# Performance work log

Hardware: AMD Instinct MI355X
Metric: run time of the kernel (lower is better)

The kernel has to match this reference:

```python
import jax, jax.numpy as jnp
import numpy as np

EMBED_DIM = 1024
N_HEADS = 16
HEAD_DIM = EMBED_DIM // N_HEADS


def setup_inputs() -> dict:
    key = jax.random.key(0)
    k_x, k_qw, k_qb, k_ow, k_ob = jax.random.split(key, 5)
    s = 1.0 / np.sqrt(EMBED_DIM)
    return {
        "x": jax.random.normal(k_x, (2, 2048, EMBED_DIM), dtype=jnp.float32),
        "qkv_w": jax.random.uniform(k_qw, (3 * EMBED_DIM, EMBED_DIM), jnp.float32, -s, s),
        "qkv_b": jax.random.uniform(k_qb, (3 * EMBED_DIM,), jnp.float32, -s, s),
        "out_w": jax.random.uniform(k_ow, (EMBED_DIM, EMBED_DIM), jnp.float32, -s, s),
        "out_b": jax.random.uniform(k_ob, (EMBED_DIM,), jnp.float32, -s, s),
    }


def reference(x, qkv_w, qkv_b, out_w, out_b):
    B, S, E = x.shape
    # fused QKV projection (torch Linear: x @ W^T + b)
    qkv = x @ qkv_w.T + qkv_b                      # [B,S,3E]
    qkv = qkv.reshape(B, S, N_HEADS, 3 * HEAD_DIM).transpose(0, 2, 1, 3)  # [B,H,S,3d]
    q, k, v = jnp.split(qkv, 3, axis=-1)           # each [B,H,S,d]
    scores = jnp.einsum("bhqd,bhkd->bhqk", q, k) / jnp.sqrt(jnp.float32(HEAD_DIM))
    weights = jax.nn.softmax(scores, axis=-1)      # [B,H,S,S]
    attn = jnp.einsum("bhqk,bhkd->bhqd", weights, v)
    attn = attn.transpose(0, 2, 1, 3).reshape(B, S, E)
    return attn @ out_w.T + out_b
```

## Files before the change

kernel.cpp:

```cpp
#include <hip/hip_runtime.h>
#include <hip/hip_bf16.h>


#define E_DIM   1024
#define NHEADS  16
#define HDIM    64
#define SEQ     2048
#define TOK     4096
#define QKV_DIM 3072
#define QSCALE_F 0.18033688011112042f

typedef __attribute__((ext_vector_type(8))) short bf16x8;
typedef __attribute__((ext_vector_type(4))) float f32x4;
typedef __attribute__((ext_vector_type(4))) int   i32x4;
typedef __attribute__((ext_vector_type(2))) int   i32x2;
typedef __attribute__((ext_vector_type(2))) __bf16 bf16x2_t;

__device__ __forceinline__ unsigned short f2bf(float x) {
    union { float f; unsigned u; } a; a.f = x;
    unsigned r = a.u + 0x7FFF + ((a.u >> 16) & 1);
    return (unsigned short)(r >> 16);
}

__device__ __forceinline__ unsigned pack2bf(float a, float b) {
#if __has_builtin(__builtin_amdgcn_cvt_pk_bf16_f32)
    union { bf16x2_t v; unsigned u; } u;
    u.v = __builtin_amdgcn_cvt_pk_bf16_f32(a, b);
    return u.u;
#else
    union { float f; unsigned u; } ua, ub; ua.f = a; ub.f = b;
    unsigned ra = ua.u + 0x7FFF + ((ua.u >> 16) & 1);
    unsigned rb = ub.u + 0x7FFF + ((ub.u >> 16) & 1);
    return (ra >> 16) | (rb & 0xFFFF0000u);
#endif
}

__device__ __forceinline__ void load_lds16(const void* g, void* l) {
    __builtin_amdgcn_global_load_lds(
        (const __attribute__((address_space(1))) void*)g,
        (__attribute__((address_space(3))) void*)l, 16, 0, 0);
}

__device__ __forceinline__ bf16x8 lds_read8(const unsigned short* p) {
    union { i32x4 i; bf16x8 b; } u;
    u.i = *(const i32x4*)p;
    return u.b;
}

__device__ __forceinline__ f32x4 mfma16(bf16x8 a, bf16x8 b, f32x4 c) {
    return __builtin_amdgcn_mfma_f32_16x16x32_bf16(a, b, c, 0, 0, 0);
}

__global__ void cast3_kernel(const float* __restrict__ a, unsigned short* __restrict__ oa, int na4,
                             const float* __restrict__ b, unsigned short* __restrict__ ob, int nb4,
                             const float* __restrict__ c, unsigned short* __restrict__ oc) {
    int i = blockIdx.x * blockDim.x + threadIdx.x;
    const float* src; unsigned short* dst; int j;
    if (i < na4)            { src = a; dst = oa; j = i; }
    else if (i < na4 + nb4) { src = b; dst = ob; j = i - na4; }
    else                    { src = c; dst = oc; j = i - na4 - nb4; }
    f32x4 v = ((const f32x4*)src)[j];
    union { i32x2 i2; unsigned u[2]; } o;
    o.u[0] = pack2bf(v.x, v.y);
    o.u[1] = pack2bf(v.z, v.w);
    ((i32x2*)dst)[j] = o.i2;
}

template<bool BF16_OUT, bool QSCALE>
__global__ __launch_bounds__(256, 2)
void gemm_bt_kernel(const unsigned short* __restrict__ A,
                    const unsigned short* __restrict__ B,
                    const float* __restrict__ bias,
                    void* __restrict__ C, int M, int N, int K) {
    __shared__ __align__(16) unsigned short As[128 * 64];
    __shared__ __align__(16) unsigned short Bs[128 * 64];

    const int tid  = threadIdx.x;
    const int wave = tid >> 6, lane = tid & 63;
    const int quad = lane >> 4, l16 = lane & 15;
    const int row0 = blockIdx.y * 128, col0 = blockIdx.x * 128;
    const int wr = (wave >> 1) * 64, wc = (wave & 1) * 64;

    f32x4 acc[4][4];
#pragma unroll
    for (int i = 0; i < 4; ++i)
#pragma unroll
        for (int j = 0; j < 4; ++j) acc[i][j] = (f32x4){0.f, 0.f, 0.f, 0.f};

    const int nkt = K >> 6;
    for (int kt = 0; kt < nkt; ++kt) {
        const int k0 = kt << 6;
#pragma unroll
        for (int i = 0; i < 4; ++i) {
            int p = i * 256 + tid;
            int r = p >> 3;
            int kc = (p & 7) ^ (r & 7);
            load_lds16(A + (size_t)(row0 + r) * K + k0 + kc * 8, &As[p * 8]);
        }
#pragma unroll
        for (int i = 0; i < 4; ++i) {
            int p = i * 256 + tid;
            int r = p >> 3;
            int kc = (p & 7) ^ (r & 7);
            load_lds16(B + (size_t)(col0 + r) * K + k0 + kc * 8, &Bs[p * 8]);
        }
        __syncthreads();

#pragma unroll
        for (int ks = 0; ks < 2; ++ks) {
            bf16x8 af[4], bfr[4];
#pragma unroll
            for (int rb = 0; rb < 4; ++rb) {
                int r_l  = wr + rb * 16 + l16;
                int phys = (ks * 4 + quad) ^ (l16 & 7);
                af[rb] = lds_read8(&As[r_l * 64 + phys * 8]);
            }
#pragma unroll
            for (int cb = 0; cb < 4; ++cb) {
                int r_l  = wc + cb * 16 + l16;
                int phys = (ks * 4 + quad) ^ (l16 & 7);
                bfr[cb] = lds_read8(&Bs[r_l * 64 + phys * 8]);
            }
#pragma unroll
            for (int rb = 0; rb < 4; ++rb)
#pragma unroll
                for (int cb = 0; cb < 4; ++cb)
                    acc[rb][cb] = mfma16(af[rb], bfr[cb], acc[rb][cb]);
        }
        __syncthreads();
    }

#pragma unroll
    for (int rb = 0; rb < 4; ++rb)
#pragma unroll
        for (int cb = 0; cb < 4; ++cb) {
            int col = col0 + wc + cb * 16 + l16;
            float bv = bias[col];
            float sc = (QSCALE && (col % 192) < 64) ? QSCALE_F : 1.0f;
#pragma unroll
            for (int reg = 0; reg < 4; ++reg) {
                int row = row0 + wr + rb * 16 + quad * 4 + reg;
                float v = (acc[rb][cb][reg] + bv) * sc;
                if (BF16_OUT)
                    ((unsigned short*)C)[(size_t)row * N + col] = f2bf(v);
                else
                    ((float*)C)[(size_t)row * N + col] = v;
            }
        }
}

__global__ __launch_bounds__(256, 2)
void gemm2_kernel(const unsigned short* __restrict__ A,
                  const unsigned short* __restrict__ B,
                  const float* __restrict__ bias,
                  float* __restrict__ C, int M, int N, int K) {
    __shared__ __align__(16) unsigned short As[128 * 64];
    __shared__ __align__(16) unsigned short Bs[64 * 64];

    const int tid  = threadIdx.x;
    const int wave = tid >> 6, lane = tid & 63;
    const int quad = lane >> 4, l16 = lane & 15;
    const int row0 = blockIdx.y * 128, col0 = blockIdx.x * 64;
    const int wr = wave * 32;

    f32x4 acc[2][4];
#pragma unroll
    for (int i = 0; i < 2; ++i)
#pragma unroll
        for (int j = 0; j < 4; ++j) acc[i][j] = (f32x4){0.f, 0.f, 0.f, 0.f};

    const int nkt = K >> 6;
    for (int kt = 0; kt < nkt; ++kt) {
        const int k0 = kt << 6;
#pragma unroll
        for (int i = 0; i < 4; ++i) {
            int p = i * 256 + tid;
            int r = p >> 3;
            int kc = (p & 7) ^ (r & 7);
            load_lds16(A + (size_t)(row0 + r) * K + k0 + kc * 8, &As[p * 8]);
        }
#pragma unroll
        for (int i = 0; i < 2; ++i) {
            int p = i * 256 + tid;
            int r = p >> 3;
            int kc = (p & 7) ^ (r & 7);
            load_lds16(B + (size_t)(col0 + r) * K + k0 + kc * 8, &Bs[p * 8]);
        }
        __syncthreads();

#pragma unroll
        for (int ks = 0; ks < 2; ++ks) {
            bf16x8 af[2], bfr[4];
#pragma unroll
            for (int rb = 0; rb < 2; ++rb) {
                int r_l  = wr + rb * 16 + l16;
                int phys = (ks * 4 + quad) ^ (l16 & 7);
                af[rb] = lds_read8(&As[r_l * 64 + phys * 8]);
            }
#pragma unroll
            for (int cb = 0; cb < 4; ++cb) {
                int r_l  = cb * 16 + l16;
                int phys = (ks * 4 + quad) ^ (l16 & 7);
                bfr[cb] = lds_read8(&Bs[r_l * 64 + phys * 8]);
            }
#pragma unroll
            for (int rb = 0; rb < 2; ++rb)
#pragma unroll
                for (int cb = 0; cb < 4; ++cb)
                    acc[rb][cb] = mfma16(af[rb], bfr[cb], acc[rb][cb]);
        }
        __syncthreads();
    }

#pragma unroll
    for (int rb = 0; rb < 2; ++rb)
#pragma unroll
        for (int cb = 0; cb < 4; ++cb) {
            int col = col0 + cb * 16 + l16;
            float bv = bias[col];
#pragma unroll
            for (int reg = 0; reg < 4; ++reg) {
                int row = row0 + wr + rb * 16 + quad * 4 + reg;
                C[(size_t)row * N + col] = acc[rb][cb][reg] + bv;
            }
        }
}

__global__ __launch_bounds__(256)
void vtrans_kernel(const unsigned short* __restrict__ qkv,
                   unsigned short* __restrict__ vT) {
    __shared__ __align__(16) unsigned short T[64 * 72];
    const int tid = threadIdx.x;
    const int bh = blockIdx.y, b = bh >> 4, h = bh & 15;
    const int s0 = blockIdx.x * 64;

    const int tok = tid & 63;
    const int ic0 = tid >> 6;
#pragma unroll
    for (int it = 0; it < 2; ++it) {
        int chunk = it * 4 + ic0;
        const unsigned short* p =
            qkv + ((size_t)(b * SEQ + s0 + tok)) * QKV_DIM + h * 192 + 128 + chunk * 8;
        union { i32x4 v; unsigned short s[8]; } va;
        va.v = *(const i32x4*)p;
#pragma unroll
        for (int j = 0; j < 8; ++j)
            T[(chunk * 8 + j) * 72 + tok] = va.s[j];
    }
    __syncthreads();

#pragma unroll
    for (int it = 0; it < 2; ++it) {
        int p = it * 256 + tid;
        int r = p >> 3, c = (p & 7) * 8;
        i32x4 v = *(const i32x4*)&T[r * 72 + c];
        *(i32x4*)&vT[((size_t)bh * 64 + r) * SEQ + s0 + c] = v;
    }
}

__global__ __launch_bounds__(256, 4)
void attn_kernel(const unsigned short* __restrict__ qkv,
                 const unsigned short* __restrict__ vT,
                 unsigned short* __restrict__ attn) {
    __shared__ __align__(16) unsigned short Ks[128 * 64];
    __shared__ __align__(16) unsigned short Vs[64 * 128];
    __shared__ __align__(16) unsigned short Ps[4][16 * 64];

    const int tid  = threadIdx.x;
    const int wave = tid >> 6, lane = tid & 63;
    const int quad = lane >> 4, l16 = lane & 15;
    const int bh = blockIdx.y;
    const int b = bh >> 4, h = bh & 15;
    const int q0 = blockIdx.x * 64;
    const size_t rowbase = (size_t)b * SEQ;
    const int qtok = q0 + wave * 16 + l16;

    int koff[2][8];
#pragma unroll
    for (int ks = 0; ks < 2; ++ks)
#pragma unroll
        for (int cb = 0; cb < 8; ++cb)
            koff[ks][cb] = (cb * 16 + l16) * 64 + (((ks * 4 + quad) ^ (l16 & 7)) * 8);
    int voff[4][4];
#pragma unroll
    for (int hk = 0; hk < 4; ++hk)
#pragma unroll
        for (int ib = 0; ib < 4; ++ib)
            voff[hk][ib] = (ib * 16 + l16) * 128 + (((hk * 4 + quad) ^ l16) * 8);
    int pwoff[4];
#pragma unroll
    for (int c4 = 0; c4 < 4; ++c4)
        pwoff[c4] = l16 * 64 + (((c4 * 2 + (quad >> 1)) ^ (l16 & 7)) * 8) + (quad & 1) * 4;
    int proff[2];
#pragma unroll
    for (int kc2 = 0; kc2 < 2; ++kc2)
        proff[kc2] = l16 * 64 + (((kc2 * 4 + quad) ^ (l16 & 7)) * 8);
    int skoff[4], svoff[4];
#pragma unroll
    for (int i = 0; i < 4; ++i) {
        int p = i * 256 + tid;
        int rk = p >> 3;
        skoff[i] = rk * QKV_DIM + ((p & 7) ^ (rk & 7)) * 8;
        int rv = p >> 4;
        svoff[i] = rv * SEQ + ((p & 15) ^ (rv & 15)) * 8;
    }

    bf16x8 qf[2];
#pragma unroll
    for (int ks = 0; ks < 2; ++ks) {
        const unsigned short* p =
            qkv + (rowbase + qtok) * QKV_DIM + h * 192 + ks * 32 + quad * 8;
        union { i32x4 i; bf16x8 b; } u;
        u.i = *(const i32x4*)p;
        qf[ks] = u.b;
    }

    f32x4 o[4];
#pragma unroll
    for (int ib = 0; ib < 4; ++ib) o[ib] = (f32x4){0.f, 0.f, 0.f, 0.f};
    float l_s = 0.f;

    for (int kt = 0; kt < SEQ / 128; ++kt) {
        const int kb = kt * 128;
        const unsigned short* kbase = qkv + (rowbase + kb) * QKV_DIM + h * 192 + 64;
        const unsigned short* vbase = vT + (size_t)bh * 64 * SEQ + kb;
#pragma unroll
        for (int i = 0; i < 4; ++i)
            load_lds16(kbase + skoff[i], &Ks[(i * 256 + tid) * 8]);
#pragma unroll
        for (int i = 0; i < 4; ++i)
            load_lds16(vbase + svoff[i], &Vs[(i * 256 + tid) * 8]);
        __syncthreads();

        f32x4 s[8];
#pragma unroll
        for (int cb = 0; cb < 8; ++cb) s[cb] = (f32x4){0.f, 0.f, 0.f, 0.f};
#pragma unroll
        for (int ks = 0; ks < 2; ++ks)
#pragma unroll
            for (int cb = 0; cb < 8; ++cb) {
                bf16x8 kf = lds_read8(&Ks[koff[ks][cb]]);
                s[cb] = mfma16(kf, qf[ks], s[cb]);
            }

        float rs = 0.f;
#pragma unroll
        for (int cb = 0; cb < 8; ++cb)
#pragma unroll
            for (int r = 0; r < 4; ++r) {
                float pv = exp2f(s[cb][r]);
                s[cb][r] = pv;
                rs += pv;
            }
        rs += __shfl_xor(rs, 16);
        rs += __shfl_xor(rs, 32);
        l_s += rs;

#pragma unroll
        for (int half = 0; half < 2; ++half) {
#pragma unroll
            for (int c4 = 0; c4 < 4; ++c4) {
                int cb = half * 4 + c4;
                i32x2 pk;
                pk.x = (int)pack2bf(s[cb][0], s[cb][1]);
                pk.y = (int)pack2bf(s[cb][2], s[cb][3]);
                *(i32x2*)&Ps[wave][pwoff[c4]] = pk;
            }
            __asm__ volatile("s_waitcnt lgkmcnt(0)" ::: "memory");
#pragma unroll
            for (int kc2 = 0; kc2 < 2; ++kc2) {
                bf16x8 pf = lds_read8(&Ps[wave][proff[kc2]]);
#pragma unroll
                for (int ib = 0; ib < 4; ++ib) {
                    bf16x8 vf = lds_read8(&Vs[voff[half * 2 + kc2][ib]]);
                    o[ib] = mfma16(pf, vf, o[ib]);
                }
            }
        }
        __syncthreads();
    }

    float il[4];
#pragma unroll
    for (int r = 0; r < 4; ++r) il[r] = 1.0f / __shfl(l_s, quad * 4 + r);
#pragma unroll
    for (int ib = 0; ib < 4; ++ib)
#pragma unroll
        for (int r = 0; r < 4; ++r) {
            int t = q0 + wave * 16 + quad * 4 + r;
            attn[(rowbase + t) * E_DIM + h * 64 + ib * 16 + l16] =
                f2bf(o[ib][r] * il[r]);
        }
}

extern "C" void kernel_launch(void* const* d_in, const int* in_sizes, int n_in,
                              void* d_out, int out_size, void* d_ws, size_t ws_size,
                              hipStream_t stream) {
    const float* x     = (const float*)d_in[0];
    const float* qkv_w = (const float*)d_in[1];
    const float* qkv_b = (const float*)d_in[2];
    const float* out_w = (const float*)d_in[3];
    const float* out_b = (const float*)d_in[4];

    char* ws = (char*)d_ws;
    unsigned short* xb   = (unsigned short*)(ws);
    unsigned short* wqkv = (unsigned short*)(ws + 8388608);
    unsigned short* wout = (unsigned short*)(ws + 14680064);
    unsigned short* qkv  = (unsigned short*)(ws + 16777216);
    unsigned short* attn = (unsigned short*)(ws + 41943040);
    unsigned short* vT   = xb;

    cast3_kernel<<<8192, 256, 0, stream>>>(x, xb, 1048576,
                                           qkv_w, wqkv, 786432,
                                           out_w, wout);

    gemm_bt_kernel<true, true><<<dim3(24, 32), 256, 0, stream>>>(
        xb, wqkv, qkv_b, (void*)qkv, TOK, QKV_DIM, E_DIM);

    vtrans_kernel<<<dim3(32, 32), 256, 0, stream>>>(qkv, vT);

    attn_kernel<<<dim3(32, 32), 256, 0, stream>>>(qkv, vT, attn);

    gemm2_kernel<<<dim3(16, 32), 256, 0, stream>>>(
        attn, wout, out_b, (float*)d_out, TOK, E_DIM, E_DIM);
}
```

Measured before the change: 216.3 us.

## Fuse V transpose into QKV GEMM epilogue and compact Q/K buffer

Result: faster. 207.7 us (-4.0%).

```diff
diff --git a/kernel.cpp b/kernel.cpp
--- a/kernel.cpp
+++ b/kernel.cpp
@@ -8,6 +8,7 @@
 #define SEQ     2048
 #define TOK     4096
 #define QKV_DIM 3072
+#define QK_STRIDE 2048
 #define QSCALE_F 0.18033688011112042f
 
 typedef __attribute__((ext_vector_type(8))) short bf16x8;
@@ -66,12 +67,13 @@
     ((i32x2*)dst)[j] = o.i2;
 }
 
-template<bool BF16_OUT, bool QSCALE>
-__global__ __launch_bounds__(256, 2)
-void gemm_bt_kernel(const unsigned short* __restrict__ A,
-                    const unsigned short* __restrict__ B,
-                    const float* __restrict__ bias,
-                    void* __restrict__ C, int M, int N, int K) {
+__global__ __launch_bounds__(256, 3)
+void gemm_qkv_kernel(const unsigned short* __restrict__ A,
+                     const unsigned short* __restrict__ B,
+                     const float* __restrict__ bias,
+                     unsigned short* __restrict__ qk,
+                     unsigned short* __restrict__ vT,
+                     int K) {
     __shared__ __align__(16) unsigned short As[128 * 64];
     __shared__ __align__(16) unsigned short Bs[128 * 64];
 
@@ -135,16 +137,27 @@
 #pragma unroll
         for (int cb = 0; cb < 4; ++cb) {
             int col = col0 + wc + cb * 16 + l16;
+            int h    = col / 192;
+            int part = col - h * 192;
             float bv = bias[col];
-            float sc = (QSCALE && (col % 192) < 64) ? QSCALE_F : 1.0f;
-#pragma unroll
-            for (int reg = 0; reg < 4; ++reg) {
-                int row = row0 + wr + rb * 16 + quad * 4 + reg;
-                float v = (acc[rb][cb][reg] + bv) * sc;
-                if (BF16_OUT)
-                    ((unsigned short*)C)[(size_t)row * N + col] = f2bf(v);
-                else
-                    ((float*)C)[(size_t)row * N + col] = v;
+            int row_b = row0 + wr + rb * 16 + quad * 4;
+            float v[4];
+#pragma unroll
+            for (int reg = 0; reg < 4; ++reg) v[reg] = acc[rb][cb][reg] + bv;
+            if (part < 128) {
+                float sc = (part < 64) ? QSCALE_F : 1.0f;
+                size_t base = (size_t)h * 128 + part;
+#pragma unroll
+                for (int reg = 0; reg < 4; ++reg)
+                    qk[(size_t)(row_b + reg) * QK_STRIDE + base] = f2bf(v[reg] * sc);
+            } else {
+                int i  = part - 128;
+                int b  = row_b >> 11;
+                int s  = row_b & 2047;
+                i32x2 pk;
+                pk.x = (int)pack2bf(v[0], v[1]);
+                pk.y = (int)pack2bf(v[2], v[3]);
+                *(i32x2*)&vT[(((size_t)(b * 16 + h)) * 64 + i) * SEQ + s] = pk;
             }
         }
 }
@@ -226,40 +239,8 @@
         }
 }
 
-__global__ __launch_bounds__(256)
-void vtrans_kernel(const unsigned short* __restrict__ qkv,
-                   unsigned short* __restrict__ vT) {
-    __shared__ __align__(16) unsigned short T[64 * 72];
-    const int tid = threadIdx.x;
-    const int bh = blockIdx.y, b = bh >> 4, h = bh & 15;
-    const int s0 = blockIdx.x * 64;
-
-    const int tok = tid & 63;
-    const int ic0 = tid >> 6;
-#pragma unroll
-    for (int it = 0; it < 2; ++it) {
-        int chunk = it * 4 + ic0;
-        const unsigned short* p =
-            qkv + ((size_t)(b * SEQ + s0 + tok)) * QKV_DIM + h * 192 + 128 + chunk * 8;
-        union { i32x4 v; unsigned short s[8]; } va;
-        va.v = *(const i32x4*)p;
-#pragma unroll
-        for (int j = 0; j < 8; ++j)
-            T[(chunk * 8 + j) * 72 + tok] = va.s[j];
-    }
-    __syncthreads();
-
-#pragma unroll
-    for (int it = 0; it < 2; ++it) {
-        int p = it * 256 + tid;
-        int r = p >> 3, c = (p & 7) * 8;
-        i32x4 v = *(const i32x4*)&T[r * 72 + c];
-        *(i32x4*)&vT[((size_t)bh * 64 + r) * SEQ + s0 + c] = v;
-    }
-}
-
 __global__ __launch_bounds__(256, 4)
-void attn_kernel(const unsigned short* __restrict__ qkv,
+void attn_kernel(const unsigned short* __restrict__ qk,
                  const unsigned short* __restrict__ vT,
                  unsigned short* __restrict__ attn) {
     __shared__ __align__(16) unsigned short Ks[128 * 64];
@@ -275,41 +256,11 @@
     const size_t rowbase = (size_t)b * SEQ;
     const int qtok = q0 + wave * 16 + l16;
 
-    int koff[2][8];
-#pragma unroll
-    for (int ks = 0; ks < 2; ++ks)
-#pragma unroll
-        for (int cb = 0; cb < 8; ++cb)
-            koff[ks][cb] = (cb * 16 + l16) * 64 + (((ks * 4 + quad) ^ (l16 & 7)) * 8);
-    int voff[4][4];
-#pragma unroll
-    for (int hk = 0; hk < 4; ++hk)
-#pragma unroll
-        for (int ib = 0; ib < 4; ++ib)
-            voff[hk][ib] = (ib * 16 + l16) * 128 + (((hk * 4 + quad) ^ l16) * 8);
-    int pwoff[4];
-#pragma unroll
-    for (int c4 = 0; c4 < 4; ++c4)
-        pwoff[c4] = l16 * 64 + (((c4 * 2 + (quad >> 1)) ^ (l16 & 7)) * 8) + (quad & 1) * 4;
-    int proff[2];
-#pragma unroll
-    for (int kc2 = 0; kc2 < 2; ++kc2)
-        proff[kc2] = l16 * 64 + (((kc2 * 4 + quad) ^ (l16 & 7)) * 8);
-    int skoff[4], svoff[4];
-#pragma unroll
-    for (int i = 0; i < 4; ++i) {
-        int p = i * 256 + tid;
-        int rk = p >> 3;
-        skoff[i] = rk * QKV_DIM + ((p & 7) ^ (rk & 7)) * 8;
-        int rv = p >> 4;
-        svoff[i] = rv * SEQ + ((p & 15) ^ (rv & 15)) * 8;
-    }
-
     bf16x8 qf[2];
 #pragma unroll
     for (int ks = 0; ks < 2; ++ks) {
         const unsigned short* p =
-            qkv + (rowbase + qtok) * QKV_DIM + h * 192 + ks * 32 + quad * 8;
+            qk + (rowbase + qtok) * QK_STRIDE + h * 128 + ks * 32 + quad * 8;
         union { i32x4 i; bf16x8 b; } u;
         u.i = *(const i32x4*)p;
         qf[ks] = u.b;
@@ -322,14 +273,22 @@
 
     for (int kt = 0; kt < SEQ / 128; ++kt) {
         const int kb = kt * 128;
-        const unsigned short* kbase = qkv + (rowbase + kb) * QKV_DIM + h * 192 + 64;
+        const unsigned short* kbase = qk + (rowbase + kb) * QK_STRIDE + h * 128 + 64;
         const unsigned short* vbase = vT + (size_t)bh * 64 * SEQ + kb;
 #pragma unroll
-        for (int i = 0; i < 4; ++i)
-            load_lds16(kbase + skoff[i], &Ks[(i * 256 + tid) * 8]);
-#pragma unroll
-        for (int i = 0; i < 4; ++i)
-            load_lds16(vbase + svoff[i], &Vs[(i * 256 + tid) * 8]);
+        for (int i = 0; i < 4; ++i) {
+            int p = i * 256 + tid;
+            int r = p >> 3;
+            int kc = (p & 7) ^ (r & 7);
+            load_lds16(kbase + r * QK_STRIDE + kc * 8, &Ks[p * 8]);
+        }
+#pragma unroll
+        for (int i = 0; i < 4; ++i) {
+            int p = i * 256 + tid;
+            int r = p >> 4;
+            int c = (p & 15) ^ (r & 15);
+            load_lds16(vbase + r * SEQ + c * 8, &Vs[p * 8]);
+        }
         __syncthreads();
 
         f32x4 s[8];
@@ -339,7 +298,8 @@
         for (int ks = 0; ks < 2; ++ks)
 #pragma unroll
             for (int cb = 0; cb < 8; ++cb) {
-                bf16x8 kf = lds_read8(&Ks[koff[ks][cb]]);
+                int phys = (ks * 4 + quad) ^ (l16 & 7);
+                bf16x8 kf = lds_read8(&Ks[(cb * 16 + l16) * 64 + phys * 8]);
                 s[cb] = mfma16(kf, qf[ks], s[cb]);
             }
 
@@ -364,15 +324,20 @@
                 i32x2 pk;
                 pk.x = (int)pack2bf(s[cb][0], s[cb][1]);
                 pk.y = (int)pack2bf(s[cb][2], s[cb][3]);
-                *(i32x2*)&Ps[wave][pwoff[c4]] = pk;
+                int off = l16 * 64 + (((c4 * 2 + (quad >> 1)) ^ (l16 & 7)) * 8)
+                        + (quad & 1) * 4;
+                *(i32x2*)&Ps[wave][off] = pk;
             }
             __asm__ volatile("s_waitcnt lgkmcnt(0)" ::: "memory");
 #pragma unroll
             for (int kc2 = 0; kc2 < 2; ++kc2) {
-                bf16x8 pf = lds_read8(&Ps[wave][proff[kc2]]);
+                bf16x8 pf = lds_read8(
+                    &Ps[wave][l16 * 64 + (((kc2 * 4 + quad) ^ (l16 & 7)) * 8)]);
 #pragma unroll
                 for (int ib = 0; ib < 4; ++ib) {
-                    bf16x8 vf = lds_read8(&Vs[voff[half * 2 + kc2][ib]]);
+                    int hk = half * 2 + kc2;
+                    int phys = (hk * 4 + quad) ^ l16;
+                    bf16x8 vf = lds_read8(&Vs[(ib * 16 + l16) * 128 + phys * 8]);
                     o[ib] = mfma16(pf, vf, o[ib]);
                 }
             }
@@ -406,20 +371,18 @@
     unsigned short* xb   = (unsigned short*)(ws);
     unsigned short* wqkv = (unsigned short*)(ws + 8388608);
     unsigned short* wout = (unsigned short*)(ws + 14680064);
-    unsigned short* qkv  = (unsigned short*)(ws + 16777216);
-    unsigned short* attn = (unsigned short*)(ws + 41943040);
-    unsigned short* vT   = xb;
+    unsigned short* qk   = (unsigned short*)(ws + 16777216);
+    unsigned short* attn = (unsigned short*)(ws + 33554432);
+    unsigned short* vT   = (unsigned short*)(ws + 41943040);
 
     cast3_kernel<<<8192, 256, 0, stream>>>(x, xb, 1048576,
                                            qkv_w, wqkv, 786432,
                                            out_w, wout);
 
-    gemm_bt_kernel<true, true><<<dim3(24, 32), 256, 0, stream>>>(
-        xb, wqkv, qkv_b, (void*)qkv, TOK, QKV_DIM, E_DIM);
-
-    vtrans_kernel<<<dim3(32, 32), 256, 0, stream>>>(qkv, vT);
-
-    attn_kernel<<<dim3(32, 32), 256, 0, stream>>>(qkv, vT, attn);
+    gemm_qkv_kernel<<<dim3(24, 32), 256, 0, stream>>>(
+        xb, wqkv, qkv_b, qk, vT, E_DIM);
+
+    attn_kernel<<<dim3(32, 32), 256, 0, stream>>>(qk, vT, attn);
 
     gemm2_kernel<<<dim3(16, 32), 256, 0, stream>>>(
         attn, wout, out_b, (float*)d_out, TOK, E_DIM, E_DIM);
```
